# Optimization experiments

Measured on AMD Instinct MI355X. Metric: run time of the kernel, lower is better.

## Reference

```python
import jax, jax.numpy as jnp
import numpy as np

NUM_VERTS = 6890
NUM_FACES = 13776
MAX_COLLISIONS = 8      # BVH(max_collisions=8)
SIGMA = 0.5             # df_cone_height
POINT2PLANE = False
PENALIZE_OUTSIDE = True
COLL_LOSS_WEIGHT = 1.0
EPS = 1e-8


def setup_inputs() -> dict:
    key = jax.random.key(0)
    k1, k2 = jax.random.split(key)
    vertices = jax.random.normal(k1, (1, NUM_VERTS, 3), dtype=jnp.float32)
    # flat face index list, as consumed by index_select(vertices, 1, faces)
    faces = jax.random.randint(k2, (NUM_FACES * 3,), 0, NUM_VERTS, dtype=jnp.int32)
    return {"vertices": vertices, "faces": faces}


def _find_collisions(triangles, faces_mat):
    """Fixed-shape emulation of the BVH broad phase.

    triangles: [B,F,3,3]. Returns collision_idxs [B, F*K, 2] int32 with -1 padding,
    pairs (receiver, intruder) whose AABBs overlap, excluding pairs of triangles
    that share a vertex (as the BVH does; this also removes self-pairs).
    """
    B, F = triangles.shape[0], triangles.shape[1]
    bbmin = triangles.min(axis=2)   # [B,F,3]
    bbmax = triangles.max(axis=2)   # [B,F,3]
    overlap = jnp.ones((B, F, F), dtype=bool)
    for a in range(3):  # fixed 3-axis loop
        lo = bbmin[:, :, a]
        hi = bbmax[:, :, a]
        overlap = overlap & (lo[:, :, None] <= hi[:, None, :]) & (lo[:, None, :] <= hi[:, :, None])
    # triangles sharing any vertex are never reported as collisions
    share = jnp.zeros((F, F), dtype=bool)
    for a in range(3):
        for b in range(3):
            share = share | (faces_mat[:, a][:, None] == faces_mat[:, b][None, :])
    valid = overlap & ~share[None]
    vals, idxs = jax.lax.top_k(valid.astype(jnp.float32), MAX_COLLISIONS)  # [B,F,K]
    intr = jnp.where(vals > 0, idxs, -1)
    recv = jnp.broadcast_to(jnp.arange(F, dtype=jnp.int32)[None, :, None], intr.shape)
    recv = jnp.where(intr >= 0, recv, -1)
    return jnp.stack([recv.reshape(B, -1), intr.reshape(B, -1)], axis=-1)  # [B,F*K,2]


def _cone_field_penalty(src_tri, pts):
    """Conical distance-field penalty (Tzionas et al.) of src triangles
    evaluated at the 3 vertices of the paired triangle.
    src_tri: [B,P,3,3] field-generating triangles; pts: [B,P,3,3] query vertices.
    Returns per-pair penalty [B,P].
    """
    e0 = src_tri[..., 1, :] - src_tri[..., 0, :]
    e1 = src_tri[..., 2, :] - src_tri[..., 0, :]
    n = jnp.cross(e0, e1)
    n = n / (jnp.linalg.norm(n, axis=-1, keepdims=True) + EPS)  # unit normal
    c = src_tri.mean(axis=-2)                                    # triangle center
    u = pts - c[..., None, :]                                    # [B,P,3,3]
    h = jnp.sum(u * n[..., None, :], axis=-1)                    # signed height [B,P,3]
    r = jnp.linalg.norm(u - h[..., None] * n[..., None, :], axis=-1)  # radial dist
    radial = jax.nn.relu(1.0 - r / SIGMA)        # linear falloff of the cone
    depth = jax.nn.relu(-h)                      # penetration depth behind the face
    if PENALIZE_OUTSIDE:
        depth = depth + jax.nn.relu(h) * jnp.exp(-h / SIGMA)  # soft outside penalty
    phi = radial * depth
    per_v = radial * h * h if POINT2PLANE else phi * phi
    return per_v.sum(axis=-1)  # sum over the 3 query vertices -> [B,P]


def reference(vertices, faces):
    B = vertices.shape[0]
    triangles = vertices[:, faces, :].reshape(B, -1, 3, 3)  # [B,F,3,3]
    faces_mat = faces.reshape(-1, 3)
    # collision search runs under no_grad in the original
    coll = _find_collisions(jax.lax.stop_gradient(triangles), faces_mat)  # [B,P,2]
    valid = (coll[..., 0] >= 0)
    recv_idx = jnp.maximum(coll[..., 0], 0)
    intr_idx = jnp.maximum(coll[..., 1], 0)
    bi = jnp.arange(B)[:, None]
    recv_tri = triangles[bi, recv_idx]  # [B,P,3,3]
    intr_tri = triangles[bi, intr_idx]  # [B,P,3,3]
    pen = _cone_field_penalty(recv_tri, intr_tri) + _cone_field_penalty(intr_tri, recv_tri)
    return COLL_LOSS_WEIGHT * jnp.sum(jnp.where(valid, pen, 0.0))
```

## Files before the change

kernel.cpp:

```cpp
#include <hip/hip_runtime.h>

#define NF   13776
#define NFP  13824
#define HALF 6888
#define KMAX 8
#define EPS  1e-8f
#define CBLK 1722

__global__ __launch_bounds__(256) void prep_kernel(
    const float* __restrict__ verts,
    const int*   __restrict__ faces,
    float4* __restrict__ tri,
    float4* __restrict__ lo4, float4* __restrict__ hi4)
{
    int f = blockIdx.x * blockDim.x + threadIdx.x;
    if (f >= NFP) return;
    if (f >= NF) {
        lo4[f] = make_float4(INFINITY, INFINITY, INFINITY, __int_as_float(-1));
        hi4[f] = make_float4(-INFINITY, -INFINITY, -INFINITY, __int_as_float(-1));
        return;
    }
    int ia = faces[3 * f + 0], ib = faces[3 * f + 1], ic = faces[3 * f + 2];
    float ax = verts[3 * ia + 0], ay = verts[3 * ia + 1], az = verts[3 * ia + 2];
    float bx = verts[3 * ib + 0], by = verts[3 * ib + 1], bz = verts[3 * ib + 2];
    float cx = verts[3 * ic + 0], cy = verts[3 * ic + 1], cz = verts[3 * ic + 2];
    tri[3 * f + 0] = make_float4(ax, ay, az, bx);
    tri[3 * f + 1] = make_float4(by, bz, cx, cy);
    tri[3 * f + 2] = make_float4(cz, 0.f, 0.f, 0.f);
    lo4[f] = make_float4(fminf(ax, fminf(bx, cx)),
                         fminf(ay, fminf(by, cy)),
                         fminf(az, fminf(bz, cz)),
                         __int_as_float((ia & 0xFFFF) | (ic << 16)));
    hi4[f] = make_float4(fmaxf(ax, fmaxf(bx, cx)),
                         fmaxf(ay, fmaxf(by, cy)),
                         fmaxf(az, fmaxf(bz, cz)),
                         __int_as_float(ib));
}

__device__ __forceinline__ float cone_pen_v(const float* s,
                                            float px, float py, float pz) {
    float e0x = s[3] - s[0], e0y = s[4] - s[1], e0z = s[5] - s[2];
    float e1x = s[6] - s[0], e1y = s[7] - s[1], e1z = s[8] - s[2];
    float nx = e0y * e1z - e0z * e1y;
    float ny = e0z * e1x - e0x * e1z;
    float nz = e0x * e1y - e0y * e1x;
    float inv = 1.0f / (sqrtf(nx * nx + ny * ny + nz * nz) + EPS);
    nx *= inv; ny *= inv; nz *= inv;
    const float third = 1.0f / 3.0f;
    float cx = (s[0] + s[3] + s[6]) * third;
    float cy = (s[1] + s[4] + s[7]) * third;
    float cz = (s[2] + s[5] + s[8]) * third;
    float ux = px - cx, uy = py - cy, uz = pz - cz;
    float h = ux * nx + uy * ny + uz * nz;
    float rx = ux - h * nx, ry = uy - h * ny, rz = uz - h * nz;
    float r = sqrtf(rx * rx + ry * ry + rz * rz);
    float radial = fmaxf(0.0f, 1.0f - 2.0f * r);
    float depth = (h < 0.0f) ? -h : h * expf(-2.0f * h);
    float phi = radial * depth;
    return phi * phi;
}

__device__ __forceinline__ bool valid_pair(
    const float4& rlo, const float4& rhi, int fa0, int fa1, int fa2,
    const float4& jlo, const float4& jhi)
{
    bool ov = (rlo.x <= jhi.x) & (jlo.x <= rhi.x)
            & (rlo.y <= jhi.y) & (jlo.y <= rhi.y)
            & (rlo.z <= jhi.z) & (jlo.z <= rhi.z);
    int w0  = __float_as_int(jlo.w);
    int fb0 = w0 & 0xFFFF;
    int fb2 = ((unsigned)w0) >> 16;
    int fb1 = __float_as_int(jhi.w);
    bool share = (fb0 == fa0) | (fb0 == fa1) | (fb0 == fa2)
               | (fb1 == fa0) | (fb1 == fa1) | (fb1 == fa2)
               | (fb2 == fa0) | (fb2 == fa1) | (fb2 == fa2);
    return ov & !share;
}

__device__ __forceinline__ void take_hits(bool valid, int base, int lane,
                                          int& nc, int& hj)
{
    unsigned long long mask = __ballot(valid);
    int cnt  = __popcll(mask);
    int take = min(cnt, KMAX - nc);
    if (lane >= nc && lane < nc + take) {
        int t = lane - nc;
        unsigned long long m = mask;
        for (int q = 0; q < t; ++q) m &= (m - 1);
        hj = base + __builtin_ctzll(m);
    }
    nc += take;
}

__device__ __forceinline__ float pen_term(const float4* __restrict__ tri,
                                          int i, int hjk, int d, int v,
                                          bool live)
{
    int jj = max(hjk, 0);
    int si = d ? jj : i;
    int qi = d ? i : jj;
    float4 s0 = tri[3 * si + 0];
    float4 s1 = tri[3 * si + 1];
    float4 s2 = tri[3 * si + 2];
    float4 q0 = tri[3 * qi + 0];
    float4 q1 = tri[3 * qi + 1];
    float4 q2 = tri[3 * qi + 2];
    float px = (v == 0) ? q0.x : ((v == 1) ? q0.w : q1.z);
    float py = (v == 0) ? q0.y : ((v == 1) ? q1.x : q1.w);
    float pz = (v == 0) ? q0.z : ((v == 1) ? q1.y : q2.x);
    float s[9] = { s0.x, s0.y, s0.z, s0.w, s1.x, s1.y, s1.z, s1.w, s2.x };
    float p = cone_pen_v(s, px, py, pz);
    return live ? p : 0.0f;
}

__global__ __launch_bounds__(256) void coll_kernel(
    const float4* __restrict__ tri,
    const float4* __restrict__ lo4, const float4* __restrict__ hi4,
    float* __restrict__ partial)
{
    const int lane = threadIdx.x & 63;
    const int wid  = threadIdx.x >> 6;
    const int gw   = (blockIdx.x * blockDim.x + threadIdx.x) >> 6;

    const int iA = gw;
    const int iB = gw + HALF;

    float4 rloA = lo4[iA], rhiA = hi4[iA];
    float4 rloB = lo4[iB], rhiB = hi4[iB];
    int wA0 = __float_as_int(rloA.w);
    int faA0 = wA0 & 0xFFFF, faA2 = ((unsigned)wA0) >> 16;
    int faA1 = __float_as_int(rhiA.w);
    int wB0 = __float_as_int(rloB.w);
    int faB0 = wB0 & 0xFFFF, faB2 = ((unsigned)wB0) >> 16;
    int faB1 = __float_as_int(rhiB.w);

    int ncA = 0, ncB = 0, hjA = -1, hjB = -1;

    {
        float4 jlo = lo4[lane], jhi = hi4[lane];
        bool vA = valid_pair(rloA, rhiA, faA0, faA1, faA2, jlo, jhi);
        bool vB = valid_pair(rloB, rhiB, faB0, faB1, faB2, jlo, jhi);
        take_hits(vA, 0, lane, ncA, hjA);
        take_hits(vB, 0, lane, ncB, hjB);
    }
    for (int base = 64; base < NFP && ncA < KMAX; base += 64) {
        float4 jlo = lo4[base + lane], jhi = hi4[base + lane];
        bool vA = valid_pair(rloA, rhiA, faA0, faA1, faA2, jlo, jhi);
        take_hits(vA, base, lane, ncA, hjA);
    }
    for (int base = 64; base < NFP && ncB < KMAX; base += 64) {
        float4 jlo = lo4[base + lane], jhi = hi4[base + lane];
        bool vB = valid_pair(rloB, rhiB, faB0, faB1, faB2, jlo, jhi);
        take_hits(vB, base, lane, ncB, hjB);
    }

    int k = lane >> 3;
    int t = lane & 7;
    int d = (t >= 3) ? 1 : 0;
    int v = t - 3 * d;
    int hjkA = __shfl(hjA, k);
    int hjkB = __shfl(hjB, k);
    bool liveT = (t < 6);
    float acc = pen_term(tri, iA, hjkA, d, v, liveT & (k < ncA))
              + pen_term(tri, iB, hjkB, d, v, liveT & (k < ncB));

#pragma unroll
    for (int off = 32; off > 0; off >>= 1) acc += __shfl_xor(acc, off);
    __shared__ float wsum[4];
    if (lane == 0) wsum[wid] = acc;
    __syncthreads();
    if (threadIdx.x == 0)
        partial[blockIdx.x] = wsum[0] + wsum[1] + wsum[2] + wsum[3];
}

__global__ __launch_bounds__(256) void reduce_kernel(
    const float* __restrict__ partial, float* __restrict__ out)
{
    float a = 0.0f;
    for (int idx = threadIdx.x; idx < CBLK; idx += 256) a += partial[idx];
#pragma unroll
    for (int off = 32; off > 0; off >>= 1) a += __shfl_xor(a, off);
    __shared__ float ws[4];
    int lane = threadIdx.x & 63, wid = threadIdx.x >> 6;
    if (lane == 0) ws[wid] = a;
    __syncthreads();
    if (threadIdx.x == 0) out[0] = ws[0] + ws[1] + ws[2] + ws[3];
}

extern "C" void kernel_launch(void* const* d_in, const int* in_sizes, int n_in,
                              void* d_out, int out_size, void* d_ws, size_t ws_size,
                              hipStream_t stream) {
    const float* verts = (const float*)d_in[0];
    const int*   faces = (const int*)d_in[1];
    float* out = (float*)d_out;

    float4* tri = (float4*)d_ws;
    float4* lo4 = tri + NFP * 3;
    float4* hi4 = lo4 + NFP;
    float*  partial = (float*)(hi4 + NFP);

    prep_kernel<<<NFP / 256, 256, 0, stream>>>(verts, faces, tri, lo4, hi4);
    coll_kernel<<<CBLK, 256, 0, stream>>>(tri, lo4, hi4, partial);
    reduce_kernel<<<1, 256, 0, stream>>>(partial, out);
}
```

Measured before the change: 67.63 us.

## Fuse triangle prep into collision kernel, gathering vertices on the fly

Removes the separate prep kernel that materialised packed triangles and AABBs, and instead has the collision kernel gather face indices and vertex coordinates directly and compute bounding boxes per candidate. This drops one kernel launch and the intermediate workspace writes and reads. In exchange, every candidate scan iteration now performs three indirect index loads and nine scattered vertex loads plus min/max work, instead of two coalesced float4 loads, repeated across all warps.

```diff
diff --git a/kernel.cpp b/kernel.cpp
--- a/kernel.cpp
+++ b/kernel.cpp
@@ -1,41 +1,10 @@
 #include <hip/hip_runtime.h>
 
 #define NF   13776
-#define NFP  13824
 #define HALF 6888
 #define KMAX 8
 #define EPS  1e-8f
 #define CBLK 1722
-
-__global__ __launch_bounds__(256) void prep_kernel(
-    const float* __restrict__ verts,
-    const int*   __restrict__ faces,
-    float4* __restrict__ tri,
-    float4* __restrict__ lo4, float4* __restrict__ hi4)
-{
-    int f = blockIdx.x * blockDim.x + threadIdx.x;
-    if (f >= NFP) return;
-    if (f >= NF) {
-        lo4[f] = make_float4(INFINITY, INFINITY, INFINITY, __int_as_float(-1));
-        hi4[f] = make_float4(-INFINITY, -INFINITY, -INFINITY, __int_as_float(-1));
-        return;
-    }
-    int ia = faces[3 * f + 0], ib = faces[3 * f + 1], ic = faces[3 * f + 2];
-    float ax = verts[3 * ia + 0], ay = verts[3 * ia + 1], az = verts[3 * ia + 2];
-    float bx = verts[3 * ib + 0], by = verts[3 * ib + 1], bz = verts[3 * ib + 2];
-    float cx = verts[3 * ic + 0], cy = verts[3 * ic + 1], cz = verts[3 * ic + 2];
-    tri[3 * f + 0] = make_float4(ax, ay, az, bx);
-    tri[3 * f + 1] = make_float4(by, bz, cx, cy);
-    tri[3 * f + 2] = make_float4(cz, 0.f, 0.f, 0.f);
-    lo4[f] = make_float4(fminf(ax, fminf(bx, cx)),
-                         fminf(ay, fminf(by, cy)),
-                         fminf(az, fminf(bz, cz)),
-                         __int_as_float((ia & 0xFFFF) | (ic << 16)));
-    hi4[f] = make_float4(fmaxf(ax, fmaxf(bx, cx)),
-                         fmaxf(ay, fmaxf(by, cy)),
-                         fmaxf(az, fmaxf(bz, cz)),
-                         __int_as_float(ib));
-}
 
 __device__ __forceinline__ float cone_pen_v(const float* s,
                                             float px, float py, float pz) {
@@ -60,21 +29,15 @@
     return phi * phi;
 }
 
-__device__ __forceinline__ bool valid_pair(
-    const float4& rlo, const float4& rhi, int fa0, int fa1, int fa2,
-    const float4& jlo, const float4& jhi)
-{
-    bool ov = (rlo.x <= jhi.x) & (jlo.x <= rhi.x)
-            & (rlo.y <= jhi.y) & (jlo.y <= rhi.y)
-            & (rlo.z <= jhi.z) & (jlo.z <= rhi.z);
-    int w0  = __float_as_int(jlo.w);
-    int fb0 = w0 & 0xFFFF;
-    int fb2 = ((unsigned)w0) >> 16;
-    int fb1 = __float_as_int(jhi.w);
-    bool share = (fb0 == fa0) | (fb0 == fa1) | (fb0 == fa2)
-               | (fb1 == fa0) | (fb1 == fa1) | (fb1 == fa2)
-               | (fb2 == fa0) | (fb2 == fa1) | (fb2 == fa2);
-    return ov & !share;
+__device__ __forceinline__ void load_tri(const float* __restrict__ verts,
+                                         const int* __restrict__ faces,
+                                         int f, float c[9],
+                                         int& i0, int& i1, int& i2)
+{
+    i0 = faces[3 * f + 0]; i1 = faces[3 * f + 1]; i2 = faces[3 * f + 2];
+    c[0] = verts[3 * i0 + 0]; c[1] = verts[3 * i0 + 1]; c[2] = verts[3 * i0 + 2];
+    c[3] = verts[3 * i1 + 0]; c[4] = verts[3 * i1 + 1]; c[5] = verts[3 * i1 + 2];
+    c[6] = verts[3 * i2 + 0]; c[7] = verts[3 * i2 + 1]; c[8] = verts[3 * i2 + 2];
 }
 
 __device__ __forceinline__ void take_hits(bool valid, int base, int lane,
@@ -92,30 +55,66 @@
     nc += take;
 }
 
-__device__ __forceinline__ float pen_term(const float4* __restrict__ tri,
-                                          int i, int hjk, int d, int v,
-                                          bool live)
+__device__ __forceinline__ float pen_term(const float* __restrict__ verts,
+                                          const int* __restrict__ faces,
+                                          const float ri[9],
+                                          int hjk, int d, int v, bool live)
 {
     int jj = max(hjk, 0);
-    int si = d ? jj : i;
-    int qi = d ? i : jj;
-    float4 s0 = tri[3 * si + 0];
-    float4 s1 = tri[3 * si + 1];
-    float4 s2 = tri[3 * si + 2];
-    float4 q0 = tri[3 * qi + 0];
-    float4 q1 = tri[3 * qi + 1];
-    float4 q2 = tri[3 * qi + 2];
-    float px = (v == 0) ? q0.x : ((v == 1) ? q0.w : q1.z);
-    float py = (v == 0) ? q0.y : ((v == 1) ? q1.x : q1.w);
-    float pz = (v == 0) ? q0.z : ((v == 1) ? q1.y : q2.x);
-    float s[9] = { s0.x, s0.y, s0.z, s0.w, s1.x, s1.y, s1.z, s1.w, s2.x };
-    float p = cone_pen_v(s, px, py, pz);
+    int b0, b1, b2;
+    float jc[9];
+    load_tri(verts, faces, jj, jc, b0, b1, b2);
+    float s[9];
+#pragma unroll
+    for (int q = 0; q < 9; ++q) s[q] = d ? jc[q] : ri[q];
+    float qx = d ? ((v == 0) ? ri[0] : (v == 1) ? ri[3] : ri[6])
+                 : ((v == 0) ? jc[0] : (v == 1) ? jc[3] : jc[6]);
+    float qy = d ? ((v == 0) ? ri[1] : (v == 1) ? ri[4] : ri[7])
+                 : ((v == 0) ? jc[1] : (v == 1) ? jc[4] : jc[7]);
+    float qz = d ? ((v == 0) ? ri[2] : (v == 1) ? ri[5] : ri[8])
+                 : ((v == 0) ? jc[2] : (v == 1) ? jc[5] : jc[8]);
+    float p = cone_pen_v(s, qx, qy, qz);
     return live ? p : 0.0f;
 }
 
+__device__ __forceinline__ void candidate(const float* __restrict__ verts,
+                                          const int* __restrict__ faces, int j,
+                                          float lo[3], float hi[3],
+                                          int& b0, int& b1, int& b2)
+{
+    if (j < NF) {
+        float c[9];
+        load_tri(verts, faces, j, c, b0, b1, b2);
+        lo[0] = fminf(c[0], fminf(c[3], c[6]));
+        lo[1] = fminf(c[1], fminf(c[4], c[7]));
+        lo[2] = fminf(c[2], fminf(c[5], c[8]));
+        hi[0] = fmaxf(c[0], fmaxf(c[3], c[6]));
+        hi[1] = fmaxf(c[1], fmaxf(c[4], c[7]));
+        hi[2] = fmaxf(c[2], fmaxf(c[5], c[8]));
+    } else {
+        lo[0] = lo[1] = lo[2] = INFINITY;
+        hi[0] = hi[1] = hi[2] = -INFINITY;
+        b0 = b1 = b2 = -1;
+    }
+}
+
+__device__ __forceinline__ bool valid_pair(const float rlo[3], const float rhi[3],
+                                           int fa0, int fa1, int fa2,
+                                           const float lo[3], const float hi[3],
+                                           int b0, int b1, int b2)
+{
+    bool ov = (rlo[0] <= hi[0]) & (lo[0] <= rhi[0])
+            & (rlo[1] <= hi[1]) & (lo[1] <= rhi[1])
+            & (rlo[2] <= hi[2]) & (lo[2] <= rhi[2]);
+    bool share = (b0 == fa0) | (b0 == fa1) | (b0 == fa2)
+               | (b1 == fa0) | (b1 == fa1) | (b1 == fa2)
+               | (b2 == fa0) | (b2 == fa1) | (b2 == fa2);
+    return ov & !share;
+}
+
 __global__ __launch_bounds__(256) void coll_kernel(
-    const float4* __restrict__ tri,
-    const float4* __restrict__ lo4, const float4* __restrict__ hi4,
+    const float* __restrict__ verts,
+    const int*   __restrict__ faces,
     float* __restrict__ partial)
 {
     const int lane = threadIdx.x & 63;
@@ -125,32 +124,43 @@
     const int iA = gw;
     const int iB = gw + HALF;
 
-    float4 rloA = lo4[iA], rhiA = hi4[iA];
-    float4 rloB = lo4[iB], rhiB = hi4[iB];
-    int wA0 = __float_as_int(rloA.w);
-    int faA0 = wA0 & 0xFFFF, faA2 = ((unsigned)wA0) >> 16;
-    int faA1 = __float_as_int(rhiA.w);
-    int wB0 = __float_as_int(rloB.w);
-    int faB0 = wB0 & 0xFFFF, faB2 = ((unsigned)wB0) >> 16;
-    int faB1 = __float_as_int(rhiB.w);
+    float rA[9], rB[9];
+    int faA0, faA1, faA2, faB0, faB1, faB2;
+    load_tri(verts, faces, iA, rA, faA0, faA1, faA2);
+    load_tri(verts, faces, iB, rB, faB0, faB1, faB2);
+    float rloA[3] = { fminf(rA[0], fminf(rA[3], rA[6])),
+                      fminf(rA[1], fminf(rA[4], rA[7])),
+                      fminf(rA[2], fminf(rA[5], rA[8])) };
+    float rhiA[3] = { fmaxf(rA[0], fmaxf(rA[3], rA[6])),
+                      fmaxf(rA[1], fmaxf(rA[4], rA[7])),
+                      fmaxf(rA[2], fmaxf(rA[5], rA[8])) };
+    float rloB[3] = { fminf(rB[0], fminf(rB[3], rB[6])),
+                      fminf(rB[1], fminf(rB[4], rB[7])),
+                      fminf(rB[2], fminf(rB[5], rB[8])) };
+    float rhiB[3] = { fmaxf(rB[0], fmaxf(rB[3], rB[6])),
+                      fmaxf(rB[1], fmaxf(rB[4], rB[7])),
+                      fmaxf(rB[2], fmaxf(rB[5], rB[8])) };
 
     int ncA = 0, ncB = 0, hjA = -1, hjB = -1;
 
     {
-        float4 jlo = lo4[lane], jhi = hi4[lane];
-        bool vA = valid_pair(rloA, rhiA, faA0, faA1, faA2, jlo, jhi);
-        bool vB = valid_pair(rloB, rhiB, faB0, faB1, faB2, jlo, jhi);
+        float lo[3], hi[3]; int b0, b1, b2;
+        candidate(verts, faces, lane, lo, hi, b0, b1, b2);
+        bool vA = valid_pair(rloA, rhiA, faA0, faA1, faA2, lo, hi, b0, b1, b2);
+        bool vB = valid_pair(rloB, rhiB, faB0, faB1, faB2, lo, hi, b0, b1, b2);
         take_hits(vA, 0, lane, ncA, hjA);
         take_hits(vB, 0, lane, ncB, hjB);
     }
-    for (int base = 64; base < NFP && ncA < KMAX; base += 64) {
-        float4 jlo = lo4[base + lane], jhi = hi4[base + lane];
-        bool vA = valid_pair(rloA, rhiA, faA0, faA1, faA2, jlo, jhi);
+    for (int base = 64; base < NF && ncA < KMAX; base += 64) {
+        float lo[3], hi[3]; int b0, b1, b2;
+        candidate(verts, faces, base + lane, lo, hi, b0, b1, b2);
+        bool vA = valid_pair(rloA, rhiA, faA0, faA1, faA2, lo, hi, b0, b1, b2);
         take_hits(vA, base, lane, ncA, hjA);
     }
-    for (int base = 64; base < NFP && ncB < KMAX; base += 64) {
-        float4 jlo = lo4[base + lane], jhi = hi4[base + lane];
-        bool vB = valid_pair(rloB, rhiB, faB0, faB1, faB2, jlo, jhi);
+    for (int base = 64; base < NF && ncB < KMAX; base += 64) {
+        float lo[3], hi[3]; int b0, b1, b2;
+        candidate(verts, faces, base + lane, lo, hi, b0, b1, b2);
+        bool vB = valid_pair(rloB, rhiB, faB0, faB1, faB2, lo, hi, b0, b1, b2);
         take_hits(vB, base, lane, ncB, hjB);
     }
 
@@ -161,8 +171,8 @@
     int hjkA = __shfl(hjA, k);
     int hjkB = __shfl(hjB, k);
     bool liveT = (t < 6);
-    float acc = pen_term(tri, iA, hjkA, d, v, liveT & (k < ncA))
-              + pen_term(tri, iB, hjkB, d, v, liveT & (k < ncB));
+    float acc = pen_term(verts, faces, rA, hjkA, d, v, liveT & (k < ncA))
+              + pen_term(verts, faces, rB, hjkB, d, v, liveT & (k < ncB));
 
 #pragma unroll
     for (int off = 32; off > 0; off >>= 1) acc += __shfl_xor(acc, off);
@@ -194,12 +204,8 @@
     const int*   faces = (const int*)d_in[1];
     float* out = (float*)d_out;
 
-    float4* tri = (float4*)d_ws;
-    float4* lo4 = tri + NFP * 3;
-    float4* hi4 = lo4 + NFP;
-    float*  partial = (float*)(hi4 + NFP);
-
-    prep_kernel<<<NFP / 256, 256, 0, stream>>>(verts, faces, tri, lo4, hi4);
-    coll_kernel<<<CBLK, 256, 0, stream>>>(tri, lo4, hi4, partial);
+    float* partial = (float*)d_ws;
+
+    coll_kernel<<<CBLK, 256, 0, stream>>>(verts, faces, partial);
     reduce_kernel<<<1, 256, 0, stream>>>(partial, out);
 }
```

Result: no change. 67.29 us (-0.5%).
